# Performance work log

Hardware: AMD Instinct MI355X
Metric: run time of the kernel (lower is better)

Reference implementation:

```python
import jax, jax.numpy as jnp
import numpy as np

TEMP = 0.1        # Similarity temperature (nonzero -> cosine path)
PAD = -100.0      # padding value used by the torch module
EPS = 1e-8        # F.cosine_similarity default eps


def setup_inputs() -> dict:
    key = jax.random.key(0)
    k1, k2, k3 = jax.random.split(key, 3)
    B, S, D = 8, 4096, 1024
    sequence_output = jax.random.normal(k1, (B, S, D), dtype=jnp.float32)
    cls = jax.random.randint(k2, (B, S), 0, 2, dtype=jnp.int32)
    is_eop = jax.random.uniform(k3, (B, S)) < 0.25
    labels = jnp.where(is_eop, cls, -100).astype(jnp.int32)
    return {"sequence_output": sequence_output, "labels": labels}


def reference(sequence_output, labels):
    # sequence_output: [B, S, D]; labels: [B, S] with -100 = ignore
    B, S, D = sequence_output.shape
    mask = labels != -100                      # [B, S]
    cnt = mask.sum(axis=1)                     # [B] eop sentence count per example
    # Stable argsort brings masked (eop) positions to the front, preserving order
    order = jnp.argsort(jnp.logical_not(mask), axis=1, stable=True)  # [B, S]
    gathered = jnp.take_along_axis(sequence_output, order[..., None], axis=1)  # [B, S, D]
    glabels = jnp.take_along_axis(labels, order, axis=1)                        # [B, S]

    pos = jnp.arange(S)[None, :]               # [1, S]
    cnt_safe = jnp.maximum(cnt, 1)[:, None]    # avoid %0 for empty examples
    nxt = (pos + 1) % cnt_safe                 # [B, S] cyclic next-sentence index
    next_vec = jnp.take_along_axis(gathered, nxt[..., None], axis=1)  # [B, S, D]

    dot = jnp.sum(gathered * next_vec, axis=-1)                 # [B, S]
    nx = jnp.linalg.norm(gathered, axis=-1)
    ny = jnp.linalg.norm(next_vec, axis=-1)
    cos = dot / jnp.maximum(nx * ny, EPS) / TEMP                # cosine / temp

    valid = pos < cnt[:, None]                                  # [B, S]
    # Torch pads to the max eop count in the batch; we pad to S (static upper
    # bound) with the same -100 fill so the math on valid slots is identical.
    cos_out = jnp.where(valid, cos, PAD)
    lab_out = jnp.where(valid, glabels, -100)
    return cos_out, lab_out
```

## Files before the change

### kernel.cpp

```cpp
#include <hip/hip_runtime.h>

#define BB 8
#define SS 4096
#define DD 1024
#define TEMP 0.1f
#define PADV -100.0f
#define EPSV 1e-8f

__global__ __launch_bounds__(1024) void compact_kernel(const int* __restrict__ labels,
                                                       int* __restrict__ idx,
                                                       int* __restrict__ cnt,
                                                       float* __restrict__ out_lab) {
    int b = blockIdx.x;
    int t = threadIdx.x;
    int lane = t & 63, wave = t >> 6;

    int4 v = ((const int4*)(labels + b * SS))[t];
    int vals[4] = {v.x, v.y, v.z, v.w};
    int mycnt = (vals[0] != -100) + (vals[1] != -100) + (vals[2] != -100) + (vals[3] != -100);

    int scan = mycnt;
#pragma unroll
    for (int off = 1; off < 64; off <<= 1) {
        int n = __shfl_up(scan, off, 64);
        if (lane >= off) scan += n;
    }

    __shared__ int wsum[16];
    if (lane == 63) wsum[wave] = scan;
    __syncthreads();

    int wbase = 0, total = 0;
#pragma unroll
    for (int w = 0; w < 16; ++w) {
        int s = wsum[w];
        wbase += (w < wave) ? s : 0;
        total += s;
    }

    if (t == 0) cnt[b] = total;

    int o = wbase + scan - mycnt;
#pragma unroll
    for (int i = 0; i < 4; ++i) {
        if (vals[i] != -100) {
            idx[b * SS + o]     = 4 * t + i;
            out_lab[b * SS + o] = (float)vals[i];
            ++o;
        }
    }
#pragma unroll
    for (int i = 0; i < 4; ++i) {
        int s = 4 * t + i;
        if (s >= total) out_lab[b * SS + s] = PADV;
    }
}

__global__ __launch_bounds__(256) void cos_kernel(const float* __restrict__ x,
                                                  const int* __restrict__ idx,
                                                  const int* __restrict__ cnt,
                                                  float* __restrict__ out_cos) {
    int b    = blockIdx.y;
    int lane = threadIdx.x & 63;
    int j    = blockIdx.x * 4 + (threadIdx.x >> 6);
    int c    = cnt[b];

    if (j >= c) {
        if (lane == 0) out_cos[b * SS + j] = PADV;
        return;
    }
    int jn = (j + 1 == c) ? 0 : (j + 1);
    const int* ib = idx + b * SS;
    const float* pa = x + ((size_t)b * SS + (size_t)ib[j])  * DD;
    const float* pb = x + ((size_t)b * SS + (size_t)ib[jn]) * DD;

    float dot = 0.f, na = 0.f, nb = 0.f;
#pragma unroll
    for (int q = 0; q < 4; ++q) {
        float4 a = *(const float4*)(pa + q * 256 + lane * 4);
        float4 w = *(const float4*)(pb + q * 256 + lane * 4);
        dot += a.x * w.x + a.y * w.y + a.z * w.z + a.w * w.w;
        na  += a.x * a.x + a.y * a.y + a.z * a.z + a.w * a.w;
        nb  += w.x * w.x + w.y * w.y + w.z * w.z + w.w * w.w;
    }
#pragma unroll
    for (int off = 32; off; off >>= 1) {
        dot += __shfl_xor(dot, off, 64);
        na  += __shfl_xor(na,  off, 64);
        nb  += __shfl_xor(nb,  off, 64);
    }
    if (lane == 0)
        out_cos[b * SS + j] = dot / fmaxf(sqrtf(na) * sqrtf(nb), EPSV) / TEMP;
}

extern "C" void kernel_launch(void* const* d_in, const int* in_sizes, int n_in,
                              void* d_out, int out_size, void* d_ws, size_t ws_size,
                              hipStream_t stream) {
    const float* seq    = (const float*)d_in[0];
    const int*   labels = (const int*)d_in[1];

    float* out_cos = (float*)d_out;
    float* out_lab = (float*)d_out + BB * SS;

    int* idx = (int*)d_ws;
    int* cnt = idx + BB * SS;

    compact_kernel<<<BB, 1024, 0, stream>>>(labels, idx, cnt, out_lab);

    dim3 grid(SS / 4, BB);
    cos_kernel<<<grid, 256, 0, stream>>>(seq, idx, cnt, out_cos);
}
```

Measured before the change: 17.91 us.

## Process eight consecutive pairs per wave, reusing each row's load and norm

Each wave now handles eight consecutive compacted positions instead of one. It carries the previous row's registers and norm forward, so every row is loaded about once rather than twice, and the grid shrinks by a factor of eight. The cost is less parallelism: far fewer waves, with serial dependent loads inside each wave, which can reduce memory-level parallelism in a kernel bound by latency and bandwidth.

```diff
diff --git a/kernel.cpp b/kernel.cpp
--- a/kernel.cpp
+++ b/kernel.cpp
@@ -62,35 +62,64 @@
                                                   float* __restrict__ out_cos) {
     int b    = blockIdx.y;
     int lane = threadIdx.x & 63;
-    int j    = blockIdx.x * 4 + (threadIdx.x >> 6);
+    int wid  = threadIdx.x >> 6;
+    int j0   = (blockIdx.x * 4 + wid) * 8;
     int c    = cnt[b];
 
-    if (j >= c) {
-        if (lane == 0) out_cos[b * SS + j] = PADV;
+    float* outp = out_cos + b * SS + j0;
+    if (j0 >= c) {
+        if (lane < 8) outp[lane] = PADV;
         return;
     }
-    int jn = (j + 1 == c) ? 0 : (j + 1);
-    const int* ib = idx + b * SS;
-    const float* pa = x + ((size_t)b * SS + (size_t)ib[j])  * DD;
-    const float* pb = x + ((size_t)b * SS + (size_t)ib[jn]) * DD;
 
-    float dot = 0.f, na = 0.f, nb = 0.f;
+    const int*   ib = idx + b * SS;
+    const float* xb = x + (size_t)b * SS * DD;
+
+    const float* pa = xb + (size_t)ib[j0] * DD;
+    float4 A0 = *(const float4*)(pa + 0 * 256 + lane * 4);
+    float4 A1 = *(const float4*)(pa + 1 * 256 + lane * 4);
+    float4 A2 = *(const float4*)(pa + 2 * 256 + lane * 4);
+    float4 A3 = *(const float4*)(pa + 3 * 256 + lane * 4);
+    float na = A0.x*A0.x + A0.y*A0.y + A0.z*A0.z + A0.w*A0.w
+             + A1.x*A1.x + A1.y*A1.y + A1.z*A1.z + A1.w*A1.w
+             + A2.x*A2.x + A2.y*A2.y + A2.z*A2.z + A2.w*A2.w
+             + A3.x*A3.x + A3.y*A3.y + A3.z*A3.z + A3.w*A3.w;
 #pragma unroll
-    for (int q = 0; q < 4; ++q) {
-        float4 a = *(const float4*)(pa + q * 256 + lane * 4);
-        float4 w = *(const float4*)(pb + q * 256 + lane * 4);
-        dot += a.x * w.x + a.y * w.y + a.z * w.z + a.w * w.w;
-        na  += a.x * a.x + a.y * a.y + a.z * a.z + a.w * a.w;
-        nb  += w.x * w.x + w.y * w.y + w.z * w.z + w.w * w.w;
+    for (int off = 32; off; off >>= 1) na += __shfl_xor(na, off, 64);
+
+    float myres = PADV;
+#pragma unroll
+    for (int k = 0; k < 8; ++k) {
+        int j = j0 + k;
+        if (j < c) {
+            int jn = (j + 1 == c) ? 0 : (j + 1);
+            const float* pb = xb + (size_t)ib[jn] * DD;
+            float4 B0 = *(const float4*)(pb + 0 * 256 + lane * 4);
+            float4 B1 = *(const float4*)(pb + 1 * 256 + lane * 4);
+            float4 B2 = *(const float4*)(pb + 2 * 256 + lane * 4);
+            float4 B3 = *(const float4*)(pb + 3 * 256 + lane * 4);
+
+            float dot = A0.x*B0.x + A0.y*B0.y + A0.z*B0.z + A0.w*B0.w
+                      + A1.x*B1.x + A1.y*B1.y + A1.z*B1.z + A1.w*B1.w
+                      + A2.x*B2.x + A2.y*B2.y + A2.z*B2.z + A2.w*B2.w
+                      + A3.x*B3.x + A3.y*B3.y + A3.z*B3.z + A3.w*B3.w;
+            float nb = B0.x*B0.x + B0.y*B0.y + B0.z*B0.z + B0.w*B0.w
+                     + B1.x*B1.x + B1.y*B1.y + B1.z*B1.z + B1.w*B1.w
+                     + B2.x*B2.x + B2.y*B2.y + B2.z*B2.z + B2.w*B2.w
+                     + B3.x*B3.x + B3.y*B3.y + B3.z*B3.z + B3.w*B3.w;
+#pragma unroll
+            for (int off = 32; off; off >>= 1) {
+                dot += __shfl_xor(dot, off, 64);
+                nb  += __shfl_xor(nb,  off, 64);
+            }
+            float r = dot / fmaxf(sqrtf(na) * sqrtf(nb), EPSV) / TEMP;
+            if (lane == k) myres = r;
+
+            A0 = B0; A1 = B1; A2 = B2; A3 = B3;
+            na = nb;
+        }
     }
-#pragma unroll
-    for (int off = 32; off; off >>= 1) {
-        dot += __shfl_xor(dot, off, 64);
-        na  += __shfl_xor(na,  off, 64);
-        nb  += __shfl_xor(nb,  off, 64);
-    }
-    if (lane == 0)
-        out_cos[b * SS + j] = dot / fmaxf(sqrtf(na) * sqrtf(nb), EPSV) / TEMP;
+    if (lane < 8) outp[lane] = myres;
 }
 
 extern "C" void kernel_launch(void* const* d_in, const int* in_sizes, int n_in,
@@ -107,6 +136,6 @@
 
     compact_kernel<<<BB, 1024, 0, stream>>>(labels, idx, cnt, out_lab);
 
-    dim3 grid(SS / 4, BB);
+    dim3 grid(SS / 32, BB);
     cos_kernel<<<grid, 256, 0, stream>>>(seq, idx, cnt, out_cos);
 }
```

Measured after the change: 22.33 us. 1.25x slower.

## Process two adjacent pairs per wave to reuse shared middle row

Applied to the files above, without the earlier changes.

Each wave now computes two consecutive cosine outputs, loading three rows instead of four, so the shared middle row and its norm are reused. This cuts global reads of the gathered rows by about a quarter. Writing the padded cos outputs moves into the compaction kernel, so the cos grid is halved and early-exit waves do no stores. In exchange each thread holds more registers, and there are fewer waves in flight to hide the random gather latency.

```diff
diff --git a/kernel.cpp b/kernel.cpp
--- a/kernel.cpp
+++ b/kernel.cpp
@@ -10,6 +10,7 @@
 __global__ __launch_bounds__(1024) void compact_kernel(const int* __restrict__ labels,
                                                        int* __restrict__ idx,
                                                        int* __restrict__ cnt,
+                                                       float* __restrict__ out_cos,
                                                        float* __restrict__ out_lab) {
     int b = blockIdx.x;
     int t = threadIdx.x;
@@ -54,6 +55,7 @@
         int s = 4 * t + i;
         if (s >= total) out_lab[b * SS + s] = PADV;
     }
+    for (int s = total + t; s < SS; s += 1024) out_cos[b * SS + s] = PADV;
 }
 
 __global__ __launch_bounds__(256) void cos_kernel(const float* __restrict__ x,
@@ -62,35 +64,54 @@
                                                   float* __restrict__ out_cos) {
     int b    = blockIdx.y;
     int lane = threadIdx.x & 63;
-    int j    = blockIdx.x * 4 + (threadIdx.x >> 6);
+    int wid  = threadIdx.x >> 6;
+    int j0   = (blockIdx.x * 4 + wid) * 2;
     int c    = cnt[b];
+    if (j0 >= c) return;
 
-    if (j >= c) {
-        if (lane == 0) out_cos[b * SS + j] = PADV;
-        return;
-    }
-    int jn = (j + 1 == c) ? 0 : (j + 1);
     const int* ib = idx + b * SS;
-    const float* pa = x + ((size_t)b * SS + (size_t)ib[j])  * DD;
-    const float* pb = x + ((size_t)b * SS + (size_t)ib[jn]) * DD;
+    int i0  = ib[j0];
+    int jn0 = (j0 + 1 == c) ? 0 : (j0 + 1);
+    int i1  = ib[jn0];
+    bool p1 = (j0 + 1 < c);
+    int jn1 = (j0 + 2 == c) ? 0 : (j0 + 2);
+    int i2  = p1 ? ib[jn1] : i1;
 
-    float dot = 0.f, na = 0.f, nb = 0.f;
+    const float* xb = x + (size_t)b * SS * DD + (size_t)lane * 4;
+    const float* pa = xb + (size_t)i0 * DD;
+    const float* pb = xb + (size_t)i1 * DD;
+    const float* pc = xb + (size_t)i2 * DD;
+
+    float4 A[4], B[4], C[4];
 #pragma unroll
     for (int q = 0; q < 4; ++q) {
-        float4 a = *(const float4*)(pa + q * 256 + lane * 4);
-        float4 w = *(const float4*)(pb + q * 256 + lane * 4);
-        dot += a.x * w.x + a.y * w.y + a.z * w.z + a.w * w.w;
-        na  += a.x * a.x + a.y * a.y + a.z * a.z + a.w * a.w;
-        nb  += w.x * w.x + w.y * w.y + w.z * w.z + w.w * w.w;
+        A[q] = *(const float4*)(pa + q * 256);
+        B[q] = *(const float4*)(pb + q * 256);
+        C[q] = *(const float4*)(pc + q * 256);
+    }
+
+    float na = 0.f, nb = 0.f, nc = 0.f, dab = 0.f, dbc = 0.f;
+#pragma unroll
+    for (int q = 0; q < 4; ++q) {
+        na  += A[q].x*A[q].x + A[q].y*A[q].y + A[q].z*A[q].z + A[q].w*A[q].w;
+        nb  += B[q].x*B[q].x + B[q].y*B[q].y + B[q].z*B[q].z + B[q].w*B[q].w;
+        nc  += C[q].x*C[q].x + C[q].y*C[q].y + C[q].z*C[q].z + C[q].w*C[q].w;
+        dab += A[q].x*B[q].x + A[q].y*B[q].y + A[q].z*B[q].z + A[q].w*B[q].w;
+        dbc += B[q].x*C[q].x + B[q].y*C[q].y + B[q].z*C[q].z + B[q].w*C[q].w;
     }
 #pragma unroll
     for (int off = 32; off; off >>= 1) {
-        dot += __shfl_xor(dot, off, 64);
         na  += __shfl_xor(na,  off, 64);
         nb  += __shfl_xor(nb,  off, 64);
+        nc  += __shfl_xor(nc,  off, 64);
+        dab += __shfl_xor(dab, off, 64);
+        dbc += __shfl_xor(dbc, off, 64);
     }
+
     if (lane == 0)
-        out_cos[b * SS + j] = dot / fmaxf(sqrtf(na) * sqrtf(nb), EPSV) / TEMP;
+        out_cos[b * SS + j0] = dab / fmaxf(sqrtf(na) * sqrtf(nb), EPSV) / TEMP;
+    if (lane == 1 && p1)
+        out_cos[b * SS + j0 + 1] = dbc / fmaxf(sqrtf(nb) * sqrtf(nc), EPSV) / TEMP;
 }
 
 extern "C" void kernel_launch(void* const* d_in, const int* in_sizes, int n_in,
@@ -105,8 +126,8 @@
     int* idx = (int*)d_ws;
     int* cnt = idx + BB * SS;
 
-    compact_kernel<<<BB, 1024, 0, stream>>>(labels, idx, cnt, out_lab);
+    compact_kernel<<<BB, 1024, 0, stream>>>(labels, idx, cnt, out_cos, out_lab);
 
-    dim3 grid(SS / 4, BB);
+    dim3 grid(SS / 8, BB);
     cos_kernel<<<grid, 256, 0, stream>>>(seq, idx, cnt, out_cos);
 }
```

New measurement: 16.88 us. 1.06x faster.
